# Kernel tuning notes

Hardware: AMD Instinct MI355X
Metric: run time of the kernel (lower is better)

The kernel has to match this reference:

```python
import jax, jax.numpy as jnp
import numpy as np

B, C, L = 4, 64, 4096

def setup_inputs() -> dict:
    key = jax.random.key(0)
    ks = jax.random.split(key, 7)
    s = 1.0 / np.sqrt(C)
    return {
        "x": jax.random.normal(ks[0], (B, C, L), dtype=jnp.float32),
        "wq": jax.random.uniform(ks[1], (C, C), jnp.float32, -s, s),
        "bq": jax.random.uniform(ks[2], (C,), jnp.float32, -s, s),
        "wk": jax.random.uniform(ks[3], (C, C), jnp.float32, -s, s),
        "bk": jax.random.uniform(ks[4], (C,), jnp.float32, -s, s),
        "wv": jax.random.uniform(ks[5], (C, C), jnp.float32, -s, s),
        "bv": jax.random.uniform(ks[6], (C,), jnp.float32, -s, s),
    }

def reference(x, wq, bq, wk, bk, wv, bv):
    # x: [B, C, L]; conv1d kernel-size-1 == per-position linear over channels.
    scale = jnp.sqrt(jnp.asarray(x.shape[1], x.dtype))
    # project and move to [B, L, C]
    q = jnp.einsum('oc,bcl->blo', wq, x) + bq  # [B, L, C]
    k = jnp.einsum('oc,bcl->blo', wk, x) + bk
    v = jnp.einsum('oc,bcl->blo', wv, x) + bv
    attn = jnp.einsum('bic,bjc->bij', q, k) / scale  # [B, L, L]
    attn = jax.nn.softmax(attn, axis=-1)
    out = jnp.einsum('bij,bjc->bic', attn, v)  # [B, L, C]
    return out.transpose(0, 2, 1) + x  # back to [B, C, L] with residual
```

## Files before the change

kernel.cpp:

```cpp
#include <hip/hip_runtime.h>
#include <hip/hip_bf16.h>

typedef float    f32x4  __attribute__((ext_vector_type(4)));
typedef float    f32x16 __attribute__((ext_vector_type(16)));
typedef short    s16x4  __attribute__((ext_vector_type(4)));
typedef short    s16x8  __attribute__((ext_vector_type(8)));
typedef unsigned u32x2  __attribute__((ext_vector_type(2)));
typedef unsigned u32x4  __attribute__((ext_vector_type(4)));
typedef __bf16   bf16x8 __attribute__((ext_vector_type(8)));

#define DEVI __device__ __forceinline__

DEVI short f2bf(float f) {
    unsigned u = __builtin_bit_cast(unsigned, f);
    u += 0x8000u;
    return (short)(u >> 16);
}
DEVI float bf2f(short s) {
    return __builtin_bit_cast(float, ((unsigned)(unsigned short)s) << 16);
}
DEVI unsigned cvt_pk_bf16(float lo, float hi) {
#if defined(__HIP_DEVICE_COMPILE__)
    unsigned r;
    asm("v_cvt_pk_bf16_f32 %0, %1, %2" : "=v"(r) : "v"(lo), "v"(hi));
    return r;
#else
    return (unsigned)(unsigned short)f2bf(lo) | ((unsigned)(unsigned short)f2bf(hi) << 16);
#endif
}

DEVI float fast_exp2(float x) {
#if defined(__HIP_DEVICE_COMPILE__) && __has_builtin(__builtin_amdgcn_exp2f)
    return __builtin_amdgcn_exp2f(x);
#else
    return exp2f(x);
#endif
}

DEVI f32x4 mfma32(s16x8 a, s16x8 b, f32x4 c) {
#if defined(__HIP_DEVICE_COMPILE__) && __has_builtin(__builtin_amdgcn_mfma_f32_16x16x32_bf16)
    return __builtin_amdgcn_mfma_f32_16x16x32_bf16(
        __builtin_bit_cast(bf16x8, a), __builtin_bit_cast(bf16x8, b), c, 0, 0, 0);
#else
    asm volatile("v_mfma_f32_16x16x32_bf16 %0, %1, %2, %0" : "+v"(c) : "v"(a), "v"(b));
    return c;
#endif
}

DEVI f32x16 mfma3216(s16x8 a, s16x8 b, f32x16 c) {
#if defined(__HIP_DEVICE_COMPILE__) && __has_builtin(__builtin_amdgcn_mfma_f32_32x32x16_bf16)
    return __builtin_amdgcn_mfma_f32_32x32x16_bf16(
        __builtin_bit_cast(bf16x8, a), __builtin_bit_cast(bf16x8, b), c, 0, 0, 0);
#else
    asm volatile("v_mfma_f32_32x32x16_bf16 %0, %1, %2, %0" : "+v"(c) : "v"(a), "v"(b));
    return c;
#endif
}

DEVI void setprio1() {
#if defined(__HIP_DEVICE_COMPILE__)
    __builtin_amdgcn_s_setprio(1);
#endif
}
DEVI void setprio0() {
#if defined(__HIP_DEVICE_COMPILE__)
    __builtin_amdgcn_s_setprio(0);
#endif
}

__global__ __launch_bounds__(512) void qkv_proj(
    const float* __restrict__ x,
    const float* __restrict__ wq, const float* __restrict__ bq,
    const float* __restrict__ wk, const float* __restrict__ bk,
    const float* __restrict__ wv, const float* __restrict__ bv,
    short* __restrict__ Qg, short* __restrict__ Kg, short* __restrict__ Vtg)
{
    __shared__ short Xt[32 * 64];

    const int b  = blockIdx.x >> 7;
    const int l0 = (blockIdx.x & 127) * 32;
    const int t  = threadIdx.x;
    const float QS = 0.18033688011112042f;

    {
        const int c  = t & 63;
        const int lh = (t >> 6) * 4;
        const float* xr = x + ((size_t)b * 64 + c) * 4096 + l0 + lh;
        const float4 x0 = *reinterpret_cast<const float4*>(xr);
        float xv[4] = {x0.x, x0.y, x0.z, x0.w};
        #pragma unroll
        for (int i = 0; i < 4; ++i) {
            const int l = lh + i;
            Xt[l * 64 + (((c >> 3) ^ (l & 7)) * 8) + (c & 7)] = f2bf(xv[i]);
        }
    }

    const int lane = t & 63, w = t >> 6;
    const int g = lane >> 4, col = lane & 15;
    const int o0 = (w & 3) * 16;
    const int h  = w >> 2;

    s16x8 wqf[2], wkf[2], wvf[2];
    #pragma unroll
    for (int kc = 0; kc < 2; ++kc) {
        const int cb = 8 * g + 32 * kc;
        const float4 q0 = *reinterpret_cast<const float4*>(wq + (o0 + col) * 64 + cb);
        const float4 q1 = *reinterpret_cast<const float4*>(wq + (o0 + col) * 64 + cb + 4);
        const float4 k0 = *reinterpret_cast<const float4*>(wk + (o0 + col) * 64 + cb);
        const float4 k1 = *reinterpret_cast<const float4*>(wk + (o0 + col) * 64 + cb + 4);
        const float4 v0 = *reinterpret_cast<const float4*>(wv + (o0 + col) * 64 + cb);
        const float4 v1 = *reinterpret_cast<const float4*>(wv + (o0 + col) * 64 + cb + 4);
        wqf[kc][0] = f2bf(q0.x * QS); wqf[kc][1] = f2bf(q0.y * QS);
        wqf[kc][2] = f2bf(q0.z * QS); wqf[kc][3] = f2bf(q0.w * QS);
        wqf[kc][4] = f2bf(q1.x * QS); wqf[kc][5] = f2bf(q1.y * QS);
        wqf[kc][6] = f2bf(q1.z * QS); wqf[kc][7] = f2bf(q1.w * QS);
        wkf[kc][0] = f2bf(k0.x); wkf[kc][1] = f2bf(k0.y);
        wkf[kc][2] = f2bf(k0.z); wkf[kc][3] = f2bf(k0.w);
        wkf[kc][4] = f2bf(k1.x); wkf[kc][5] = f2bf(k1.y);
        wkf[kc][6] = f2bf(k1.z); wkf[kc][7] = f2bf(k1.w);
        wvf[kc][0] = f2bf(v0.x); wvf[kc][1] = f2bf(v0.y);
        wvf[kc][2] = f2bf(v0.z); wvf[kc][3] = f2bf(v0.w);
        wvf[kc][4] = f2bf(v1.x); wvf[kc][5] = f2bf(v1.y);
        wvf[kc][6] = f2bf(v1.z); wvf[kc][7] = f2bf(v1.w);
    }
    const f32x4 bq4 = *reinterpret_cast<const f32x4*>(bq + o0 + 4 * g);
    const f32x4 bk4 = *reinterpret_cast<const f32x4*>(bk + o0 + 4 * g);
    const float bvs = bv[o0 + col];

    __syncthreads();

    {
        const int row = h * 16 + col;
        const s16x8 xf0 = *reinterpret_cast<const s16x8*>(
            &Xt[row * 64 + ((g ^ (row & 7)) * 8)]);
        const s16x8 xf1 = *reinterpret_cast<const s16x8*>(
            &Xt[row * 64 + (((g + 4) ^ (row & 7)) * 8)]);

        f32x4 qa = bq4 * QS;
        qa = mfma32(wqf[0], xf0, qa);
        qa = mfma32(wqf[1], xf1, qa);
        f32x4 ka = bk4;
        ka = mfma32(wkf[0], xf0, ka);
        ka = mfma32(wkf[1], xf1, ka);
        f32x4 va = {bvs, bvs, bvs, bvs};
        va = mfma32(xf0, wvf[0], va);
        va = mfma32(xf1, wvf[1], va);

        s16x4 qs, ks;
        #pragma unroll
        for (int r = 0; r < 4; ++r) { qs[r] = f2bf(qa[r]); ks[r] = f2bf(ka[r]); }
        const size_t qkbase = ((size_t)b * 4096 + l0 + row) * 64 + o0 + 4 * g;
        *reinterpret_cast<s16x4*>(Qg + qkbase) = qs;
        *reinterpret_cast<s16x4*>(Kg + qkbase) = ks;

        s16x4 vs;
        #pragma unroll
        for (int r = 0; r < 4; ++r) vs[r] = f2bf(va[r]);
        *reinterpret_cast<s16x4*>(
            Vtg + ((size_t)b * 64 + o0 + col) * 4096 + l0 + h * 16 + 4 * g) = vs;
    }
}

__global__ __launch_bounds__(512, 2) void attn_fused(
    const short* __restrict__ Qg, const short* __restrict__ Kg,
    const short* __restrict__ Vtg, const float* __restrict__ x,
    float* __restrict__ out)
{
    __shared__ short SM[65536];

    const int bid = blockIdx.x;
    const int wid = (bid & 7) * 32 + (bid >> 3);
    const int b   = wid >> 6;
    const int qt  = wid & 63;

    const int t    = threadIdx.x;
    const int w    = t >> 6;
    const int lane = t & 63;
    const int qi   = lane & 31;
    const int hi   = lane >> 5;
    const int rx   = qi & 7;
    const int kw   = w & 3;
    const int qw   = w >> 2;

    const int qglob = qt * 64 + qw * 32 + qi;

    s16x8 qf[4];
    {
        const short* qp = Qg + ((size_t)b * 4096 + qglob) * 64 + 8 * hi;
        qf[0] = *reinterpret_cast<const s16x8*>(qp);
        qf[1] = *reinterpret_cast<const s16x8*>(qp + 16);
        qf[2] = *reinterpret_cast<const s16x8*>(qp + 32);
        qf[3] = *reinterpret_cast<const s16x8*>(qp + 48);
    }

    const short* Kb = Kg  + (size_t)b * 4096 * 64;
    const short* Vb = Vtg + (size_t)b * 64 * 4096;

    const int ks   = t >> 7;
    const int tl   = t & 127;
    const int slot = tl & 7;
    const int r0   = tl >> 3;
    const int r7   = r0 & 7;
    int kdoff[4], vdoff0[4], vdoff1[4];
    {
        const int pg0 = ((2 * slot) & 60) | (slot & 1);
        const int pg1 = pg0 | 2;
        const int vs0 = (((pg0 >> 1) ^ r7) << 3) + ((pg0 & 1) << 2);
        const int vs1 = (((pg1 >> 1) ^ r7) << 3) + ((pg1 & 1) << 2);
        #pragma unroll
        for (int c = 0; c < 4; ++c) {
            const int row = r0 + 16 * c;
            kdoff[c]  = row * 64 + ((slot ^ r7) * 8);
            vdoff0[c] = row * 64 + vs0;
            vdoff1[c] = row * 64 + vs1;
        }
    }
    const short* kgb = Kb + ((size_t)ks * 1024 + r0) * 64 + slot * 8;
    const short* vgb = Vb + (size_t)r0 * 4096 + ks * 1024 + slot * 8;

    short* Kst = SM + ks * 2 * 4096;
    short* Vst = SM + 32768 + ks * 2 * 4096;

    s16x8 kpre[4], vpre[4];
    #pragma unroll
    for (int c = 0; c < 4; ++c) {
        kpre[c] = *reinterpret_cast<const s16x8*>(kgb + (size_t)(16 * c) * 64);
        vpre[c] = *reinterpret_cast<const s16x8*>(vgb + (size_t)(16 * c) * 4096);
    }
    #pragma unroll
    for (int c = 0; c < 4; ++c) {
        *reinterpret_cast<s16x8*>(&Kst[kdoff[c]]) = kpre[c];
        s16x4 vlo = {vpre[c][0], vpre[c][1], vpre[c][2], vpre[c][3]};
        s16x4 vhi = {vpre[c][4], vpre[c][5], vpre[c][6], vpre[c][7]};
        *reinterpret_cast<s16x4*>(&Vst[vdoff0[c]]) = vlo;
        *reinterpret_cast<s16x4*>(&Vst[vdoff1[c]]) = vhi;
    }
    __syncthreads();

    f32x16 oacc0 = {}, oacc1 = {};
    float lsum = 0.0f;

    const short* Kc = SM + kw * 2 * 4096;
    const short* Vc = SM + 32768 + kw * 2 * 4096;

    #pragma unroll 2
    for (int tt = 0; tt < 16; ++tt) {
        const int cur = tt & 1;
        const short* Kl = Kc + cur * 4096;
        const short* Vl = Vc + cur * 4096;

        if (tt < 15) {
            #pragma unroll
            for (int c = 0; c < 4; ++c) {
                kpre[c] = *reinterpret_cast<const s16x8*>(
                    kgb + (size_t)(tt + 1) * 4096 + (size_t)(16 * c) * 64);
                vpre[c] = *reinterpret_cast<const s16x8*>(
                    vgb + (tt + 1) * 64 + (size_t)(16 * c) * 4096);
            }
        }

        #pragma unroll
        for (int jb = 0; jb < 2; ++jb) {
            const short* kr  = Kl + (jb * 32 + qi) * 64;
            const short* vr0 = Vl + qi * 64;
            const short* vr1 = Vl + (32 + qi) * 64;

            f32x16 S = {};
            setprio1();
            #pragma unroll
            for (int m = 0; m < 4; ++m) {
                const s16x8 a = *reinterpret_cast<const s16x8*>(
                    kr + (((2 * m + hi) ^ rx) * 8));
                S = mfma3216(a, qf[m], S);
            }
            setprio0();

            const int sA0 = ((4 * jb + 0 + hi) ^ rx) * 8;
            const int sA1 = ((4 * jb + 2 + hi) ^ rx) * 8;
            const s16x8 va00 = *reinterpret_cast<const s16x8*>(vr0 + sA0);
            const s16x8 va10 = *reinterpret_cast<const s16x8*>(vr1 + sA0);
            const s16x8 va01 = *reinterpret_cast<const s16x8*>(vr0 + sA1);
            const s16x8 va11 = *reinterpret_cast<const s16x8*>(vr1 + sA1);

            unsigned Pu[8];
            float ps = 0.0f;
            #pragma unroll
            for (int i = 0; i < 8; ++i) {
                const float e0 = fast_exp2(S[2 * i]);
                const float e1 = fast_exp2(S[2 * i + 1]);
                ps += e0 + e1;
                Pu[i] = cvt_pk_bf16(e0, e1);
            }
            lsum += ps;
            const u32x4 w0 = {Pu[0], Pu[1], Pu[2], Pu[3]};
            const u32x4 w1 = {Pu[4], Pu[5], Pu[6], Pu[7]};

            setprio1();
            oacc0 = mfma3216(va00, __builtin_bit_cast(s16x8, w0), oacc0);
            oacc1 = mfma3216(va10, __builtin_bit_cast(s16x8, w0), oacc1);
            oacc0 = mfma3216(va01, __builtin_bit_cast(s16x8, w1), oacc0);
            oacc1 = mfma3216(va11, __builtin_bit_cast(s16x8, w1), oacc1);
            setprio0();
        }

        if (tt < 15) {
            short* Kd = Kst + (cur ^ 1) * 4096;
            short* Vd = Vst + (cur ^ 1) * 4096;
            #pragma unroll
            for (int c = 0; c < 4; ++c) {
                *reinterpret_cast<s16x8*>(&Kd[kdoff[c]]) = kpre[c];
                s16x4 vlo = {vpre[c][0], vpre[c][1], vpre[c][2], vpre[c][3]};
                s16x4 vhi = {vpre[c][4], vpre[c][5], vpre[c][6], vpre[c][7]};
                *reinterpret_cast<s16x4*>(&Vd[vdoff0[c]]) = vlo;
                *reinterpret_cast<s16x4*>(&Vd[vdoff1[c]]) = vhi;
            }
        }
        __syncthreads();
    }

    const float ltot = lsum + __shfl_xor(lsum, 32);

    float* Of = reinterpret_cast<float*>(SM);
    float* Lf = Of + 8 * 32 * 65;
    {
        const int rowb = (kw * 64 + qw * 32 + qi) * 65;
        #pragma unroll
        for (int db = 0; db < 2; ++db) {
            const f32x16 oa = db ? oacc1 : oacc0;
            #pragma unroll
            for (int r = 0; r < 16; ++r) {
                const int d = (r & 3) + 8 * (r >> 2) + 4 * hi + 32 * db;
                Of[rowb + d] = oa[r];
            }
        }
        if (hi == 0) Lf[kw * 64 + qw * 32 + qi] = ltot;
    }
    __syncthreads();

    {
        const int d  = t >> 3;
        const int q8 = (t & 7) * 8;
        float res[8];
        #pragma unroll
        for (int i = 0; i < 8; ++i) {
            const int rb = q8 + i;
            const float L = Lf[rb] + Lf[64 + rb] + Lf[128 + rb] + Lf[192 + rb];
            const float o = Of[(rb)       * 65 + d] + Of[(64 + rb)  * 65 + d] +
                            Of[(128 + rb) * 65 + d] + Of[(192 + rb) * 65 + d];
            res[i] = o / L;
        }
        const size_t ob = ((size_t)b * 64 + d) * 4096 + qt * 64 + q8;
        const float4 x0 = *reinterpret_cast<const float4*>(x + ob);
        const float4 x1 = *reinterpret_cast<const float4*>(x + ob + 4);
        float4 o0 = {res[0] + x0.x, res[1] + x0.y, res[2] + x0.z, res[3] + x0.w};
        float4 o1 = {res[4] + x1.x, res[5] + x1.y, res[6] + x1.z, res[7] + x1.w};
        *reinterpret_cast<float4*>(out + ob)     = o0;
        *reinterpret_cast<float4*>(out + ob + 4) = o1;
    }
}

extern "C" void kernel_launch(void* const* d_in, const int* in_sizes, int n_in,
                              void* d_out, int out_size, void* d_ws, size_t ws_size,
                              hipStream_t stream) {
    const float* x  = (const float*)d_in[0];
    const float* wq = (const float*)d_in[1];
    const float* bq = (const float*)d_in[2];
    const float* wk = (const float*)d_in[3];
    const float* bk = (const float*)d_in[4];
    const float* wv = (const float*)d_in[5];
    const float* bv = (const float*)d_in[6];
    float* out = (float*)d_out;

    short* Qg  = reinterpret_cast<short*>(d_ws);
    short* Kg  = Qg  + (size_t)4 * 4096 * 64;
    short* Vtg = Kg  + (size_t)4 * 4096 * 64;

    qkv_proj<<<dim3(512), dim3(512), 0, stream>>>(x, wq, bq, wk, bk, wv, bv, Qg, Kg, Vtg);
    attn_fused<<<dim3(256), dim3(512), 0, stream>>>(Qg, Kg, Vtg, x, out);
}
```

Baseline: 42.50 us.

## Give each wave private double-buffered K/V staging and drop per-tile block barriers

Replaces the block-cooperative K/V staging, which needed a __syncthreads every tile, with per-wave private LDS buffers. Each wave now loads and double-buffers its own 32-key K/V tiles, in 32 iterations instead of 16, so no block barrier is needed inside the main loop. V uses a padded row stride of 40 in place of the XOR swizzle. In exchange, the two query waves that share a key split each load the same K/V data, doubling global/L2 traffic. LDS grows to 144 KB per block, which likely limits residency to one block per CU despite the launch bound of 2.

```diff
diff --git a/kernel.cpp b/kernel.cpp
--- a/kernel.cpp
+++ b/kernel.cpp
@@ -5,7 +5,6 @@
 typedef float    f32x16 __attribute__((ext_vector_type(16)));
 typedef short    s16x4  __attribute__((ext_vector_type(4)));
 typedef short    s16x8  __attribute__((ext_vector_type(8)));
-typedef unsigned u32x2  __attribute__((ext_vector_type(2)));
 typedef unsigned u32x4  __attribute__((ext_vector_type(4)));
 typedef __bf16   bf16x8 __attribute__((ext_vector_type(8)));
 
@@ -166,7 +165,7 @@
     const short* __restrict__ Vtg, const float* __restrict__ x,
     float* __restrict__ out)
 {
-    __shared__ short SM[65536];
+    __shared__ short SM[73728];
 
     const int bid = blockIdx.x;
     const int wid = (bid & 7) * 32 + (bid >> 3);
@@ -196,116 +195,103 @@
     const short* Kb = Kg  + (size_t)b * 4096 * 64;
     const short* Vb = Vtg + (size_t)b * 64 * 4096;
 
-    const int ks   = t >> 7;
-    const int tl   = t & 127;
-    const int slot = tl & 7;
-    const int r0   = tl >> 3;
-    const int r7   = r0 & 7;
+    const int r0k = lane >> 3;
+    const int sk  = lane & 7;
+    const int r0v = lane >> 2;
+    const int sv  = lane & 3;
+
+    short* Kbuf = SM + w * 9216;
+    short* Vbuf = SM + w * 9216 + 4096;
+
     int kdoff[4], vdoff0[4], vdoff1[4];
     {
-        const int pg0 = ((2 * slot) & 60) | (slot & 1);
-        const int pg1 = pg0 | 2;
-        const int vs0 = (((pg0 >> 1) ^ r7) << 3) + ((pg0 & 1) << 2);
-        const int vs1 = (((pg1 >> 1) ^ r7) << 3) + ((pg1 & 1) << 2);
+        const int dest0 = ((sv & 2) << 1) | (sv & 1);
+        const int dest1 = dest0 | 2;
         #pragma unroll
         for (int c = 0; c < 4; ++c) {
-            const int row = r0 + 16 * c;
-            kdoff[c]  = row * 64 + ((slot ^ r7) * 8);
-            vdoff0[c] = row * 64 + vs0;
-            vdoff1[c] = row * 64 + vs1;
-        }
-    }
-    const short* kgb = Kb + ((size_t)ks * 1024 + r0) * 64 + slot * 8;
-    const short* vgb = Vb + (size_t)r0 * 4096 + ks * 1024 + slot * 8;
-
-    short* Kst = SM + ks * 2 * 4096;
-    short* Vst = SM + 32768 + ks * 2 * 4096;
+            kdoff[c]  = (c * 8 + r0k) * 64 + ((sk ^ (r0k & 7)) * 8);
+            vdoff0[c] = (c * 16 + r0v) * 40 + dest0 * 4;
+            vdoff1[c] = (c * 16 + r0v) * 40 + dest1 * 4;
+        }
+    }
+    const short* kgb = Kb + ((size_t)kw * 1024 + r0k) * 64 + sk * 8;
+    const short* vgb = Vb + (size_t)r0v * 4096 + kw * 1024 + sv * 8;
 
     s16x8 kpre[4], vpre[4];
     #pragma unroll
     for (int c = 0; c < 4; ++c) {
-        kpre[c] = *reinterpret_cast<const s16x8*>(kgb + (size_t)(16 * c) * 64);
-        vpre[c] = *reinterpret_cast<const s16x8*>(vgb + (size_t)(16 * c) * 4096);
+        kpre[c] = *reinterpret_cast<const s16x8*>(kgb + c * 512);
+        vpre[c] = *reinterpret_cast<const s16x8*>(vgb + (size_t)c * 65536);
     }
     #pragma unroll
     for (int c = 0; c < 4; ++c) {
-        *reinterpret_cast<s16x8*>(&Kst[kdoff[c]]) = kpre[c];
+        *reinterpret_cast<s16x8*>(&Kbuf[kdoff[c]]) = kpre[c];
         s16x4 vlo = {vpre[c][0], vpre[c][1], vpre[c][2], vpre[c][3]};
         s16x4 vhi = {vpre[c][4], vpre[c][5], vpre[c][6], vpre[c][7]};
-        *reinterpret_cast<s16x4*>(&Vst[vdoff0[c]]) = vlo;
-        *reinterpret_cast<s16x4*>(&Vst[vdoff1[c]]) = vhi;
-    }
-    __syncthreads();
+        *reinterpret_cast<s16x4*>(&Vbuf[vdoff0[c]]) = vlo;
+        *reinterpret_cast<s16x4*>(&Vbuf[vdoff1[c]]) = vhi;
+    }
 
     f32x16 oacc0 = {}, oacc1 = {};
     float lsum = 0.0f;
 
-    const short* Kc = SM + kw * 2 * 4096;
-    const short* Vc = SM + 32768 + kw * 2 * 4096;
-
     #pragma unroll 2
-    for (int tt = 0; tt < 16; ++tt) {
+    for (int tt = 0; tt < 32; ++tt) {
         const int cur = tt & 1;
-        const short* Kl = Kc + cur * 4096;
-        const short* Vl = Vc + cur * 4096;
-
-        if (tt < 15) {
+        const short* Kl = Kbuf + cur * 2048;
+        const short* Vl = Vbuf + cur * 2560;
+
+        if (tt < 31) {
             #pragma unroll
             for (int c = 0; c < 4; ++c) {
                 kpre[c] = *reinterpret_cast<const s16x8*>(
-                    kgb + (size_t)(tt + 1) * 4096 + (size_t)(16 * c) * 64);
+                    kgb + (tt + 1) * 2048 + c * 512);
                 vpre[c] = *reinterpret_cast<const s16x8*>(
-                    vgb + (tt + 1) * 64 + (size_t)(16 * c) * 4096);
+                    vgb + (tt + 1) * 32 + (size_t)c * 65536);
             }
         }
 
-        #pragma unroll
-        for (int jb = 0; jb < 2; ++jb) {
-            const short* kr  = Kl + (jb * 32 + qi) * 64;
-            const short* vr0 = Vl + qi * 64;
-            const short* vr1 = Vl + (32 + qi) * 64;
-
-            f32x16 S = {};
-            setprio1();
-            #pragma unroll
-            for (int m = 0; m < 4; ++m) {
-                const s16x8 a = *reinterpret_cast<const s16x8*>(
-                    kr + (((2 * m + hi) ^ rx) * 8));
-                S = mfma3216(a, qf[m], S);
-            }
-            setprio0();
-
-            const int sA0 = ((4 * jb + 0 + hi) ^ rx) * 8;
-            const int sA1 = ((4 * jb + 2 + hi) ^ rx) * 8;
-            const s16x8 va00 = *reinterpret_cast<const s16x8*>(vr0 + sA0);
-            const s16x8 va10 = *reinterpret_cast<const s16x8*>(vr1 + sA0);
-            const s16x8 va01 = *reinterpret_cast<const s16x8*>(vr0 + sA1);
-            const s16x8 va11 = *reinterpret_cast<const s16x8*>(vr1 + sA1);
-
-            unsigned Pu[8];
-            float ps = 0.0f;
-            #pragma unroll
-            for (int i = 0; i < 8; ++i) {
-                const float e0 = fast_exp2(S[2 * i]);
-                const float e1 = fast_exp2(S[2 * i + 1]);
-                ps += e0 + e1;
-                Pu[i] = cvt_pk_bf16(e0, e1);
-            }
-            lsum += ps;
-            const u32x4 w0 = {Pu[0], Pu[1], Pu[2], Pu[3]};
-            const u32x4 w1 = {Pu[4], Pu[5], Pu[6], Pu[7]};
-
-            setprio1();
-            oacc0 = mfma3216(va00, __builtin_bit_cast(s16x8, w0), oacc0);
-            oacc1 = mfma3216(va10, __builtin_bit_cast(s16x8, w0), oacc1);
-            oacc0 = mfma3216(va01, __builtin_bit_cast(s16x8, w1), oacc0);
-            oacc1 = mfma3216(va11, __builtin_bit_cast(s16x8, w1), oacc1);
-            setprio0();
-        }
-
-        if (tt < 15) {
-            short* Kd = Kst + (cur ^ 1) * 4096;
-            short* Vd = Vst + (cur ^ 1) * 4096;
+        const short* kr = Kl + qi * 64;
+        f32x16 S = {};
+        setprio1();
+        #pragma unroll
+        for (int m = 0; m < 4; ++m) {
+            const s16x8 a = *reinterpret_cast<const s16x8*>(
+                kr + (((2 * m + hi) ^ rx) * 8));
+            S = mfma3216(a, qf[m], S);
+        }
+        setprio0();
+
+        const short* vr0 = Vl + qi * 40;
+        const short* vr1 = Vl + (32 + qi) * 40;
+        const s16x8 va00 = *reinterpret_cast<const s16x8*>(vr0 + hi * 8);
+        const s16x8 va10 = *reinterpret_cast<const s16x8*>(vr1 + hi * 8);
+        const s16x8 va01 = *reinterpret_cast<const s16x8*>(vr0 + (2 + hi) * 8);
+        const s16x8 va11 = *reinterpret_cast<const s16x8*>(vr1 + (2 + hi) * 8);
+
+        unsigned Pu[8];
+        float ps = 0.0f;
+        #pragma unroll
+        for (int i = 0; i < 8; ++i) {
+            const float e0 = fast_exp2(S[2 * i]);
+            const float e1 = fast_exp2(S[2 * i + 1]);
+            ps += e0 + e1;
+            Pu[i] = cvt_pk_bf16(e0, e1);
+        }
+        lsum += ps;
+        const u32x4 w0 = {Pu[0], Pu[1], Pu[2], Pu[3]};
+        const u32x4 w1 = {Pu[4], Pu[5], Pu[6], Pu[7]};
+
+        setprio1();
+        oacc0 = mfma3216(va00, __builtin_bit_cast(s16x8, w0), oacc0);
+        oacc1 = mfma3216(va10, __builtin_bit_cast(s16x8, w0), oacc1);
+        oacc0 = mfma3216(va01, __builtin_bit_cast(s16x8, w1), oacc0);
+        oacc1 = mfma3216(va11, __builtin_bit_cast(s16x8, w1), oacc1);
+        setprio0();
+
+        if (tt < 31) {
+            short* Kd = Kbuf + (cur ^ 1) * 2048;
+            short* Vd = Vbuf + (cur ^ 1) * 2560;
             #pragma unroll
             for (int c = 0; c < 4; ++c) {
                 *reinterpret_cast<s16x8*>(&Kd[kdoff[c]]) = kpre[c];
@@ -315,13 +301,13 @@
                 *reinterpret_cast<s16x4*>(&Vd[vdoff1[c]]) = vhi;
             }
         }
-        __syncthreads();
     }
 
     const float ltot = lsum + __shfl_xor(lsum, 32);
 
+    __syncthreads();
     float* Of = reinterpret_cast<float*>(SM);
-    float* Lf = Of + 8 * 32 * 65;
+    float* Lf = Of + 256 * 65;
     {
         const int rowb = (kw * 64 + qw * 32 + qi) * 65;
         #pragma unroll
```

After: 48.29 us. +13.6%, slower.

## Pre-swizzle K/V tiles in projection and stream them via direct global-to-LDS loads

Applied to the files above, without the earlier changes.

The projection kernel now writes K and V into per-64-row tiles already laid out in the swizzled LDS format the attention kernel expects. The attention kernel then copies each tile with contiguous global_load_lds transfers instead of loading into registers and scattering into shared memory. This is meant to cut VGPR pressure, per-thread address arithmetic and the LDS store instructions in the main loop. The cost is scattered, narrow global writes in the projection kernel, and a dependence on the async LDS-load builtin being available and waited on correctly at the barrier.

```diff
diff --git a/kernel.cpp b/kernel.cpp
--- a/kernel.cpp
+++ b/kernel.cpp
@@ -5,7 +5,6 @@
 typedef float    f32x16 __attribute__((ext_vector_type(16)));
 typedef short    s16x4  __attribute__((ext_vector_type(4)));
 typedef short    s16x8  __attribute__((ext_vector_type(8)));
-typedef unsigned u32x2  __attribute__((ext_vector_type(2)));
 typedef unsigned u32x4  __attribute__((ext_vector_type(4)));
 typedef __bf16   bf16x8 __attribute__((ext_vector_type(8)));
 
@@ -15,9 +14,6 @@
     unsigned u = __builtin_bit_cast(unsigned, f);
     u += 0x8000u;
     return (short)(u >> 16);
-}
-DEVI float bf2f(short s) {
-    return __builtin_bit_cast(float, ((unsigned)(unsigned short)s) << 16);
 }
 DEVI unsigned cvt_pk_bf16(float lo, float hi) {
 #if defined(__HIP_DEVICE_COMPILE__)
@@ -68,12 +64,23 @@
 #endif
 }
 
+DEVI void gld_lds16(const short* g, short* ldsb, int lane) {
+#if defined(__HIP_DEVICE_COMPILE__) && __has_builtin(__builtin_amdgcn_global_load_lds)
+    __builtin_amdgcn_global_load_lds(
+        (const __attribute__((address_space(1))) void*)g,
+        (__attribute__((address_space(3))) void*)ldsb, 16, 0, 0);
+#else
+    *reinterpret_cast<s16x8*>(ldsb + lane * 8) =
+        *reinterpret_cast<const s16x8*>(g);
+#endif
+}
+
 __global__ __launch_bounds__(512) void qkv_proj(
     const float* __restrict__ x,
     const float* __restrict__ wq, const float* __restrict__ bq,
     const float* __restrict__ wk, const float* __restrict__ bk,
     const float* __restrict__ wv, const float* __restrict__ bv,
-    short* __restrict__ Qg, short* __restrict__ Kg, short* __restrict__ Vtg)
+    short* __restrict__ Qg, short* __restrict__ Kp, short* __restrict__ Vp)
 {
     __shared__ short Xt[32 * 64];
 
@@ -149,21 +156,39 @@
         s16x4 qs, ks;
         #pragma unroll
         for (int r = 0; r < 4; ++r) { qs[r] = f2bf(qa[r]); ks[r] = f2bf(ka[r]); }
-        const size_t qkbase = ((size_t)b * 4096 + l0 + row) * 64 + o0 + 4 * g;
-        *reinterpret_cast<s16x4*>(Qg + qkbase) = qs;
-        *reinterpret_cast<s16x4*>(Kg + qkbase) = ks;
-
-        s16x4 vs;
-        #pragma unroll
-        for (int r = 0; r < 4; ++r) vs[r] = f2bf(va[r]);
-        *reinterpret_cast<s16x4*>(
-            Vtg + ((size_t)b * 64 + o0 + col) * 4096 + l0 + h * 16 + 4 * g) = vs;
+
+        const int l  = l0 + row;
+        const int d0 = o0 + 4 * g;
+        *reinterpret_cast<s16x4*>(Qg + ((size_t)b * 4096 + l) * 64 + d0) = qs;
+
+        {
+            const int T  = l >> 6;
+            const int rj = l & 63;
+            const int off = rj * 64 + (((d0 >> 3) ^ (rj & 7)) << 3)
+                          + ((d0 >> 2) & 1) * 4;
+            *reinterpret_cast<s16x4*>(
+                Kp + ((size_t)(b * 64 + T)) * 4096 + off) = ks;
+        }
+
+        {
+            s16x4 vs;
+            #pragma unroll
+            for (int r = 0; r < 4; ++r) vs[r] = f2bf(va[r]);
+            const int dV  = o0 + col;
+            const int jgl = l0 + h * 16 + 4 * g;
+            const int TV  = jgl >> 6;
+            const int g4  = (jgl & 63) >> 2;
+            const int p   = (g4 & 12) | ((g4 >> 1) & 1) | ((g4 & 1) << 1);
+            const int off = dV * 64 + (((p >> 1) ^ (dV & 7)) << 3) + (p & 1) * 4;
+            *reinterpret_cast<s16x4*>(
+                Vp + ((size_t)(b * 64 + TV)) * 4096 + off) = vs;
+        }
     }
 }
 
 __global__ __launch_bounds__(512, 2) void attn_fused(
-    const short* __restrict__ Qg, const short* __restrict__ Kg,
-    const short* __restrict__ Vtg, const float* __restrict__ x,
+    const short* __restrict__ Qg, const short* __restrict__ Kp,
+    const short* __restrict__ Vp, const float* __restrict__ x,
     float* __restrict__ out)
 {
     __shared__ short SM[65536];
@@ -193,70 +218,37 @@
         qf[3] = *reinterpret_cast<const s16x8*>(qp + 48);
     }
 
-    const short* Kb = Kg  + (size_t)b * 4096 * 64;
-    const short* Vb = Vtg + (size_t)b * 64 * 4096;
-
-    const int ks   = t >> 7;
-    const int tl   = t & 127;
-    const int slot = tl & 7;
-    const int r0   = tl >> 3;
-    const int r7   = r0 & 7;
-    int kdoff[4], vdoff0[4], vdoff1[4];
-    {
-        const int pg0 = ((2 * slot) & 60) | (slot & 1);
-        const int pg1 = pg0 | 2;
-        const int vs0 = (((pg0 >> 1) ^ r7) << 3) + ((pg0 & 1) << 2);
-        const int vs1 = (((pg1 >> 1) ^ r7) << 3) + ((pg1 & 1) << 2);
-        #pragma unroll
-        for (int c = 0; c < 4; ++c) {
-            const int row = r0 + 16 * c;
-            kdoff[c]  = row * 64 + ((slot ^ r7) * 8);
-            vdoff0[c] = row * 64 + vs0;
-            vdoff1[c] = row * 64 + vs1;
-        }
-    }
-    const short* kgb = Kb + ((size_t)ks * 1024 + r0) * 64 + slot * 8;
-    const short* vgb = Vb + (size_t)r0 * 4096 + ks * 1024 + slot * 8;
-
-    short* Kst = SM + ks * 2 * 4096;
-    short* Vst = SM + 32768 + ks * 2 * 4096;
-
-    s16x8 kpre[4], vpre[4];
-    #pragma unroll
-    for (int c = 0; c < 4; ++c) {
-        kpre[c] = *reinterpret_cast<const s16x8*>(kgb + (size_t)(16 * c) * 64);
-        vpre[c] = *reinterpret_cast<const s16x8*>(vgb + (size_t)(16 * c) * 4096);
-    }
-    #pragma unroll
-    for (int c = 0; c < 4; ++c) {
-        *reinterpret_cast<s16x8*>(&Kst[kdoff[c]]) = kpre[c];
-        s16x4 vlo = {vpre[c][0], vpre[c][1], vpre[c][2], vpre[c][3]};
-        s16x4 vhi = {vpre[c][4], vpre[c][5], vpre[c][6], vpre[c][7]};
-        *reinterpret_cast<s16x4*>(&Vst[vdoff0[c]]) = vlo;
-        *reinterpret_cast<s16x4*>(&Vst[vdoff1[c]]) = vhi;
+    const int ds = w & 3;
+    const short* srcb = (w < 4)
+        ? (Kp + ((size_t)(b * 64 + ds * 16)) * 4096 + lane * 8)
+        : (Vp + ((size_t)(b * 64 + ds * 16)) * 4096 + lane * 8);
+    short* ldsb = (w < 4) ? (SM + (ds * 2) * 4096)
+                          : (SM + 32768 + (ds * 2) * 4096);
+
+    {
+        const short* s0 = srcb;
+        short* l0p = ldsb;
+        #pragma unroll
+        for (int i = 0; i < 8; ++i)
+            gld_lds16(s0 + i * 512, l0p + i * 512, lane);
     }
     __syncthreads();
 
     f32x16 oacc0 = {}, oacc1 = {};
     float lsum = 0.0f;
-
-    const short* Kc = SM + kw * 2 * 4096;
-    const short* Vc = SM + 32768 + kw * 2 * 4096;
 
     #pragma unroll 2
     for (int tt = 0; tt < 16; ++tt) {
         const int cur = tt & 1;
-        const short* Kl = Kc + cur * 4096;
-        const short* Vl = Vc + cur * 4096;
+        const short* Kl = SM + (kw * 2 + cur) * 4096;
+        const short* Vl = SM + 32768 + (kw * 2 + cur) * 4096;
 
         if (tt < 15) {
-            #pragma unroll
-            for (int c = 0; c < 4; ++c) {
-                kpre[c] = *reinterpret_cast<const s16x8*>(
-                    kgb + (size_t)(tt + 1) * 4096 + (size_t)(16 * c) * 64);
-                vpre[c] = *reinterpret_cast<const s16x8*>(
-                    vgb + (tt + 1) * 64 + (size_t)(16 * c) * 4096);
-            }
+            const short* s1 = srcb + (size_t)(tt + 1) * 4096;
+            short* l1p = ldsb + (cur ^ 1) * 4096;
+            #pragma unroll
+            for (int i = 0; i < 8; ++i)
+                gld_lds16(s1 + i * 512, l1p + i * 512, lane);
         }
 
         #pragma unroll
@@ -303,25 +295,13 @@
             setprio0();
         }
 
-        if (tt < 15) {
-            short* Kd = Kst + (cur ^ 1) * 4096;
-            short* Vd = Vst + (cur ^ 1) * 4096;
-            #pragma unroll
-            for (int c = 0; c < 4; ++c) {
-                *reinterpret_cast<s16x8*>(&Kd[kdoff[c]]) = kpre[c];
-                s16x4 vlo = {vpre[c][0], vpre[c][1], vpre[c][2], vpre[c][3]};
-                s16x4 vhi = {vpre[c][4], vpre[c][5], vpre[c][6], vpre[c][7]};
-                *reinterpret_cast<s16x4*>(&Vd[vdoff0[c]]) = vlo;
-                *reinterpret_cast<s16x4*>(&Vd[vdoff1[c]]) = vhi;
-            }
-        }
         __syncthreads();
     }
 
     const float ltot = lsum + __shfl_xor(lsum, 32);
 
     float* Of = reinterpret_cast<float*>(SM);
-    float* Lf = Of + 8 * 32 * 65;
+    float* Lf = Of + 256 * 65;
     {
         const int rowb = (kw * 64 + qw * 32 + qi) * 65;
         #pragma unroll
@@ -371,10 +351,10 @@
     const float* bv = (const float*)d_in[6];
     float* out = (float*)d_out;
 
-    short* Qg  = reinterpret_cast<short*>(d_ws);
-    short* Kg  = Qg  + (size_t)4 * 4096 * 64;
-    short* Vtg = Kg  + (size_t)4 * 4096 * 64;
-
-    qkv_proj<<<dim3(512), dim3(512), 0, stream>>>(x, wq, bq, wk, bk, wv, bv, Qg, Kg, Vtg);
-    attn_fused<<<dim3(256), dim3(512), 0, stream>>>(Qg, Kg, Vtg, x, out);
-}
+    short* Qg = reinterpret_cast<short*>(d_ws);
+    short* Kp = Qg + (size_t)4 * 4096 * 64;
+    short* Vp = Kp + (size_t)4 * 4096 * 64;
+
+    qkv_proj<<<dim3(512), dim3(512), 0, stream>>>(x, wq, bq, wk, bk, wv, bv, Qg, Kp, Vp);
+    attn_fused<<<dim3(256), dim3(512), 0, stream>>>(Qg, Kp, Vp, x, out);
+}
```

Measured after the change: 39.18 us. -7.8%, faster.
